# Performance work log

Hardware: AMD Instinct MI355X
Metric: run time of the kernel (lower is better)

The kernel has to match this reference:

```python
import jax, jax.numpy as jnp
import numpy as np

CELL = 4  # 2 ** cell_2_pow, cell_2_pow = 2
EPS = 1e-5


def conv2d(x, w, b):
    # 3x3 conv, padding 1, NCHW / OIHW
    y = jax.lax.conv_general_dilated(
        x, w, window_strides=(1, 1), padding=((1, 1), (1, 1)),
        dimension_numbers=('NCHW', 'OIHW', 'NCHW'))
    return y + b[None, :, None, None]


def setup_inputs() -> dict:
    key = jax.random.key(0)
    ks = jax.random.split(key, 4)
    B, Cc, H, W = 8, 128, 512, 512
    nh, nw = H // CELL, W // CELL  # ctrl spatial must be padded_img / cell_sz
    return dict(
        image_pipe=jax.random.normal(ks[0], (B, 6, H, W), jnp.float32),
        ctrl_pipe=jax.random.normal(ks[1], (B, Cc, nh, nw), jnp.float32),
        w1=jax.random.normal(ks[2], (50, Cc, 3, 3), jnp.float32) * 0.03,
        b1=jnp.zeros((50,), jnp.float32),
        gamma=jnp.ones((50,), jnp.float32),
        beta=jnp.zeros((50,), jnp.float32),
        mean=jnp.zeros((50,), jnp.float32),
        var=jnp.ones((50,), jnp.float32),
        w2=jax.random.normal(ks[3], (18, 50, 3, 3), jnp.float32) * 0.05,
        b2=jnp.zeros((18,), jnp.float32),
    )


def reference(image_pipe, ctrl_pipe, w1, b1, gamma, beta, mean, var, w2, b2):
    cs = CELL
    B, C6, H, W = image_pipe.shape
    # conv_condense: Conv(Cc->50) -> ReLU -> BatchNorm2d(50, inference) -> Conv(50->18)
    h = jax.nn.relu(conv2d(ctrl_pipe, w1, b1))
    scale = gamma * jax.lax.rsqrt(var + EPS)
    h = (h - mean[None, :, None, None]) * scale[None, :, None, None] + beta[None, :, None, None]
    cond = conv2d(h, w2, b2)  # [B, 18, nh, nw]
    nh, nw = cond.shape[-2], cond.shape[-1]

    padH = (-H) % cs
    padW = (-W) % cs
    rH, rW = H + padH, W + padW
    # F.pad(img, (cell, padW+cell, cell, padH+cell)): left/right then top/bottom
    img = jnp.pad(image_pipe, ((0, 0), (0, 0), (cs, padH + cs), (cs, padW + cs)))

    # 9 cell-strided shifted views; torch loop order: i over width (outer), j over height (inner)
    stack = jnp.stack(
        [img[:, :, j * cs:j * cs + rH, i * cs:i * cs + rW]
         for i in range(3) for j in range(3)], axis=-1)  # [B, 6, rH, rW, 9]
    stack = stack.reshape(B, 2, 3, rH, rW, 9)  # 2 groups of 3 channels

    # per-pixel dynamic 9-tap weights, constant within each cs x cs cell
    wts = cond.reshape(B, 2, 9, nh, nw)
    wts = jnp.repeat(jnp.repeat(wts, cs, axis=3), cs, axis=4)  # [B, 2, 9, rH, rW]

    out = jnp.einsum('bgchwk,bgkhw->bgchw', stack, wts)  # weighted neighborhood sum
    out = out.reshape(B, 6, rH, rW)[:, :, :H, :W]
    return out
```

## Files before the change

### kernel.cpp

```cpp
#include <hip/hip_runtime.h>

typedef __attribute__((ext_vector_type(8))) short short8;
typedef __attribute__((ext_vector_type(4))) float floatx4;

__device__ __forceinline__ unsigned short f2bf(float f) {
    union { float f; unsigned int u; } v; v.f = f;
    unsigned int r = (v.u + 0x7fffu + ((v.u >> 16) & 1u)) >> 16;
    return (unsigned short)r;
}

__global__ __launch_bounds__(256) void transpose_kernel(
    const float* __restrict__ ctrl, unsigned short* __restrict__ ctrlT)
{
    __shared__ unsigned short tile[64 * 66];
    const int t = threadIdx.x;
    const int x0 = blockIdx.x * 64, ci0 = blockIdx.y * 64;
    const int b = blockIdx.z >> 7, y = blockIdx.z & 127;
#pragma unroll
    for (int it = 0; it < 4; it++) {
        int ci_l = it * 16 + (t >> 4);
        int x_l = (t & 15) * 4;
        const float4 v = *(const float4*)&ctrl[(((size_t)b * 128 + ci0 + ci_l) * 128 + y) * 128 + x0 + x_l];
        tile[(x_l + 0) * 66 + ci_l] = f2bf(v.x);
        tile[(x_l + 1) * 66 + ci_l] = f2bf(v.y);
        tile[(x_l + 2) * 66 + ci_l] = f2bf(v.z);
        tile[(x_l + 3) * 66 + ci_l] = f2bf(v.w);
    }
    __syncthreads();
#pragma unroll
    for (int it = 0; it < 2; it++) {
        int x_l = it * 32 + (t >> 3);
        int ci_l = (t & 7) * 8;
        const unsigned int* p = (const unsigned int*)&tile[x_l * 66 + ci_l];
        uint4 u = make_uint4(p[0], p[1], p[2], p[3]);
        *(uint4*)&ctrlT[(((size_t)b * 128 + y) * 128 + x0 + x_l) * 128 + ci0 + ci_l] = u;
    }
}

__global__ __launch_bounds__(256) void prep_w_kernel(
    const float* __restrict__ w1, const float* __restrict__ w2,
    unsigned short* __restrict__ w1p, unsigned short* __restrict__ w2p)
{
    int i = blockIdx.x * 256 + threadIdx.x;
    if (i < 4 * 9 * 64 * 32) {
        int ci = i & 31; int t2 = i >> 5; int co = t2 & 63; int t3 = t2 >> 6;
        int tap = t3 % 9; int c4 = t3 / 9;
        float v = 0.f;
        if (co < 50) v = w1[((size_t)co * 128 + c4 * 32 + ci) * 9 + tap];
        w1p[i] = f2bf(v);
    } else {
        int j = i - 4 * 9 * 64 * 32;
        int ci = j & 31; int t2 = j >> 5; int co = t2 & 31; int t3 = t2 >> 5;
        int tap = t3 % 9; int c4 = t3 / 9;
        int cig = c4 * 32 + ci;
        float v = 0.f;
        if (co < 18 && cig < 50) v = w2[((size_t)co * 50 + cig) * 9 + tap];
        w2p[j] = f2bf(v);
    }
}

__global__ __launch_bounds__(256) void conv1_mfma(
    const unsigned short* __restrict__ xT, const unsigned short* __restrict__ w1p,
    const float* __restrict__ b1, const float* __restrict__ gamma,
    const float* __restrict__ beta, const float* __restrict__ mean,
    const float* __restrict__ var, unsigned short* __restrict__ h)
{
    __shared__ unsigned short in_s[324 * 40];
    __shared__ unsigned short w_s[9 * 64 * 40];
    const int tid = threadIdx.x;
    const int x0 = blockIdx.x * 16, y0 = blockIdx.y * 16, b = blockIdx.z;
    const int wid = tid >> 6, lane = tid & 63;
    const int ln = lane & 15, q = lane >> 4;

    floatx4 acc[4][4];
#pragma unroll
    for (int mt = 0; mt < 4; mt++)
#pragma unroll
        for (int nt = 0; nt < 4; nt++) acc[mt][nt] = (floatx4)(0.f);

    uint4 in_r[6], w_r[9];
    auto load_in = [&](int c4) {
#pragma unroll
        for (int k = 0; k < 6; k++) {
            int i = tid + k * 256;
            if (i < 1296) {
                int p = i >> 2, g = i & 3;
                int gy = y0 + p / 18 - 1, gx = x0 + p % 18 - 1;
                in_r[k] = make_uint4(0, 0, 0, 0);
                if (gy >= 0 && gy < 128 && gx >= 0 && gx < 128)
                    in_r[k] = *(const uint4*)&xT[(((size_t)b * 128 + gy) * 128 + gx) * 128 + c4 * 32 + g * 8];
            }
        }
    };
    auto load_w = [&](int c4) {
#pragma unroll
        for (int it = 0; it < 9; it++) {
            int f = it * 256 + tid;
            int g = f & 3, co = (f >> 2) & 63, tap = f >> 8;
            w_r[it] = *(const uint4*)&w1p[(((size_t)c4 * 9 + tap) * 64 + co) * 32 + g * 8];
        }
    };
    auto write_in = [&]() {
#pragma unroll
        for (int k = 0; k < 6; k++) {
            int i = tid + k * 256;
            if (i < 1296) {
                int p = i >> 2, g = i & 3;
                *(uint4*)&in_s[p * 40 + g * 8] = in_r[k];
            }
        }
    };
    auto write_w = [&]() {
#pragma unroll
        for (int it = 0; it < 9; it++) {
            int f = it * 256 + tid;
            int g = f & 3, co = (f >> 2) & 63, tap = f >> 8;
            *(uint4*)&w_s[(tap * 64 + co) * 40 + g * 8] = w_r[it];
        }
    };

    load_in(0); load_w(0);
    write_in(); write_w();
    __syncthreads();

    for (int c4 = 0; c4 < 4; c4++) {
        if (c4 < 3) { load_in(c4 + 1); load_w(c4 + 1); }
#pragma unroll
        for (int tap = 0; tap < 9; tap++) {
            const int dy = tap / 3, dx = tap % 3;
            short8 a[4];
#pragma unroll
            for (int mt = 0; mt < 4; mt++)
                a[mt] = *(const short8*)&in_s[((wid * 4 + mt + dy) * 18 + ln + dx) * 40 + q * 8];
#pragma unroll
            for (int nt = 0; nt < 4; nt++) {
                short8 bf = *(const short8*)&w_s[(tap * 64 + nt * 16 + ln) * 40 + q * 8];
#pragma unroll
                for (int mt = 0; mt < 4; mt++)
                    acc[mt][nt] = __builtin_amdgcn_mfma_f32_16x16x32_bf16(a[mt], bf, acc[mt][nt], 0, 0, 0);
            }
        }
        __syncthreads();
        if (c4 < 3) { write_in(); write_w(); __syncthreads(); }
    }

#pragma unroll
    for (int nt = 0; nt < 4; nt++) {
        int co = nt * 16 + ln;
        bool real = co < 50;
        float sc = 0.f, mn = 0.f, bt = 0.f, bs = 0.f;
        if (real) {
            sc = gamma[co] * rsqrtf(var[co] + 1e-5f);
            mn = mean[co]; bt = beta[co]; bs = b1[co];
        }
#pragma unroll
        for (int mt = 0; mt < 4; mt++) {
            int gy = y0 + wid * 4 + mt;
#pragma unroll
            for (int r = 0; r < 4; r++) {
                int px = q * 4 + r;
                float v = 0.f;
                if (real) {
                    float tv = fmaxf(acc[mt][nt][r] + bs, 0.f);
                    v = (tv - mn) * sc + bt;
                }
                h[(((size_t)b * 128 + gy) * 128 + x0 + px) * 64 + co] = f2bf(v);
            }
        }
    }
}

__global__ __launch_bounds__(256) void conv2_mfma(
    const unsigned short* __restrict__ hT, const unsigned short* __restrict__ w2p,
    const float* __restrict__ b2, float* __restrict__ cond)
{
    __shared__ unsigned short in_s[324 * 40];
    __shared__ unsigned short w_s[2][9 * 32 * 40];
    const int tid = threadIdx.x;
    const int x0 = blockIdx.x * 16, y0 = blockIdx.y * 16, b = blockIdx.z;
    const int wid = tid >> 6, lane = tid & 63;
    const int ln = lane & 15, q = lane >> 4;

    floatx4 acc[4][2];
#pragma unroll
    for (int mt = 0; mt < 4; mt++)
#pragma unroll
        for (int nt = 0; nt < 2; nt++) acc[mt][nt] = (floatx4)(0.f);

    uint4 in_r[6];
    auto load_in = [&](int c4) {
#pragma unroll
        for (int k = 0; k < 6; k++) {
            int i = tid + k * 256;
            if (i < 1296) {
                int p = i >> 2, g = i & 3;
                int gy = y0 + p / 18 - 1, gx = x0 + p % 18 - 1;
                in_r[k] = make_uint4(0, 0, 0, 0);
                if (gy >= 0 && gy < 128 && gx >= 0 && gx < 128)
                    in_r[k] = *(const uint4*)&hT[(((size_t)b * 128 + gy) * 128 + gx) * 64 + c4 * 32 + g * 8];
            }
        }
    };
    auto write_in = [&]() {
#pragma unroll
        for (int k = 0; k < 6; k++) {
            int i = tid + k * 256;
            if (i < 1296) {
                int p = i >> 2, g = i & 3;
                *(uint4*)&in_s[p * 40 + g * 8] = in_r[k];
            }
        }
    };

    load_in(0);
#pragma unroll
    for (int it = 0; it < 9; it++) {
        int f = it * 256 + tid;
        int c4w = f >= 1152 ? 1 : 0;
        int f2 = f - c4w * 1152;
        int g = f2 & 3, co = (f2 >> 2) & 31, tap = f2 >> 7;
        uint4 v = *(const uint4*)&w2p[(((size_t)c4w * 9 + tap) * 32 + co) * 32 + g * 8];
        *(uint4*)&w_s[c4w][(tap * 32 + co) * 40 + g * 8] = v;
    }
    write_in();
    __syncthreads();

    for (int c4 = 0; c4 < 2; c4++) {
        if (c4 < 1) load_in(1);
#pragma unroll
        for (int tap = 0; tap < 9; tap++) {
            const int dy = tap / 3, dx = tap % 3;
            short8 a[4];
#pragma unroll
            for (int mt = 0; mt < 4; mt++)
                a[mt] = *(const short8*)&in_s[((wid * 4 + mt + dy) * 18 + ln + dx) * 40 + q * 8];
#pragma unroll
            for (int nt = 0; nt < 2; nt++) {
                short8 bf = *(const short8*)&w_s[c4][(tap * 32 + nt * 16 + ln) * 40 + q * 8];
#pragma unroll
                for (int mt = 0; mt < 4; mt++)
                    acc[mt][nt] = __builtin_amdgcn_mfma_f32_16x16x32_bf16(a[mt], bf, acc[mt][nt], 0, 0, 0);
            }
        }
        if (c4 < 1) {
            __syncthreads();
            write_in();
            __syncthreads();
        }
    }

#pragma unroll
    for (int nt = 0; nt < 2; nt++) {
        int co = nt * 16 + ln;
        if (co < 18) {
            float bs = b2[co];
            int gch = co / 9, k = co % 9;
            int iw = k / 3, jy = k % 3;
#pragma unroll
            for (int mt = 0; mt < 4; mt++) {
                int gy = y0 + wid * 4 + mt;
#pragma unroll
                for (int r = 0; r < 4; r++) {
                    int px = q * 4 + r;
                    cond[((((size_t)b * 2 + gch) * 128 + gy) * 128 + (x0 + px)) * 12 + jy * 4 + iw]
                        = acc[mt][nt][r] + bs;
                }
            }
        }
    }
}

__global__ __launch_bounds__(256) void apply_kernel(
    const float* __restrict__ img, const float* __restrict__ cond,
    float* __restrict__ out)
{
    const int hwid = blockIdx.x;
    const int lid = (hwid & 7) * 512 + (hwid >> 3);
    const int bx = lid & 1, by = (lid >> 1) & 127, bz = lid >> 8;

    const int tid = threadIdx.x;
    const int xl = tid & 63, s = tid >> 6;
    const int x4 = bx * 64 + xl;
    const int o = by * 4 + s;
    const int b = bz >> 1, g = bz & 1;
    const int xo = x4 * 4;

    const float* cw = &cond[((((size_t)b * 2 + g) * 128 + by) * 128 + x4) * 12];
    float4 w0 = *(const float4*)&cw[0];
    float4 w1 = *(const float4*)&cw[4];
    float4 w2 = *(const float4*)&cw[8];

    float4 C[3][3], L[3][3], R[3][3];
    const bool lok = (x4 > 0), rok_x = (x4 < 127);
#pragma unroll
    for (int jy = 0; jy < 3; jy++) {
        const int r = o - 4 + 4 * jy;
        const bool rk = (r >= 0) && (r < 512);
#pragma unroll
        for (int cc = 0; cc < 3; cc++) {
            C[jy][cc] = make_float4(0.f, 0.f, 0.f, 0.f);
            L[jy][cc] = make_float4(0.f, 0.f, 0.f, 0.f);
            R[jy][cc] = make_float4(0.f, 0.f, 0.f, 0.f);
            if (rk) {
                const float* rp = &img[((((size_t)b * 6 + g * 3 + cc) * 512) + r) * 512];
                C[jy][cc] = *(const float4*)&rp[xo];
                if (lok)   L[jy][cc] = *(const float4*)&rp[xo - 4];
                if (rok_x) R[jy][cc] = *(const float4*)&rp[xo + 4];
            }
        }
    }

    float4 acc[3];
#pragma unroll
    for (int cc = 0; cc < 3; cc++) acc[cc] = make_float4(0.f, 0.f, 0.f, 0.f);

#pragma unroll
    for (int jy = 0; jy < 3; jy++) {
        const float4 wj = (jy == 0) ? w0 : (jy == 1) ? w1 : w2;
#pragma unroll
        for (int cc = 0; cc < 3; cc++) {
            const float4 l = L[jy][cc], c = C[jy][cc], r = R[jy][cc];
            acc[cc].x += l.x * wj.x + c.x * wj.y + r.x * wj.z;
            acc[cc].y += l.y * wj.x + c.y * wj.y + r.y * wj.z;
            acc[cc].z += l.z * wj.x + c.z * wj.y + r.z * wj.z;
            acc[cc].w += l.w * wj.x + c.w * wj.y + r.w * wj.z;
        }
    }

#pragma unroll
    for (int cc = 0; cc < 3; cc++)
        *(float4*)&out[((((size_t)b * 6 + g * 3 + cc) * 512) + o) * 512 + xo] = acc[cc];
}

extern "C" void kernel_launch(void* const* d_in, const int* in_sizes, int n_in,
                              void* d_out, int out_size, void* d_ws, size_t ws_size,
                              hipStream_t stream)
{
    const float* img   = (const float*)d_in[0];
    const float* ctrl  = (const float*)d_in[1];
    const float* w1    = (const float*)d_in[2];
    const float* b1    = (const float*)d_in[3];
    const float* gamma = (const float*)d_in[4];
    const float* beta  = (const float*)d_in[5];
    const float* mean  = (const float*)d_in[6];
    const float* var   = (const float*)d_in[7];
    const float* w2    = (const float*)d_in[8];
    const float* b2    = (const float*)d_in[9];
    float* out = (float*)d_out;

    char* ws = (char*)d_ws;
    unsigned short* ctrlT = (unsigned short*)ws;
    float*          cond  = (float*)ws;
    unsigned short* hbuf  = (unsigned short*)(ws + 33554432);
    unsigned short* w1p   = (unsigned short*)(ws + 50331648);
    unsigned short* w2p   = (unsigned short*)(ws + 50479104);

    transpose_kernel<<<dim3(2, 2, 1024), 256, 0, stream>>>(ctrl, ctrlT);
    prep_w_kernel<<<360, 256, 0, stream>>>(w1, w2, w1p, w2p);
    conv1_mfma<<<dim3(8, 8, 8), 256, 0, stream>>>(ctrlT, w1p, b1, gamma, beta, mean, var, hbuf);
    conv2_mfma<<<dim3(8, 8, 8), 256, 0, stream>>>(hbuf, w2p, b2, cond);
    apply_kernel<<<4096, 256, 0, stream>>>(img, cond, out);
}
```

Baseline: 243.6 us.

## Use direct global-to-LDS loads with pre-padded halo buffers in conv kernels

```diff
diff --git a/kernel.cpp b/kernel.cpp
--- a/kernel.cpp
+++ b/kernel.cpp
@@ -7,6 +7,12 @@
     union { float f; unsigned int u; } v; v.f = f;
     unsigned int r = (v.u + 0x7fffu + ((v.u >> 16) & 1u)) >> 16;
     return (unsigned short)r;
+}
+
+__device__ __forceinline__ void gload_lds16(const void* g, void* l) {
+    __builtin_amdgcn_global_load_lds(
+        (const __attribute__((address_space(1))) unsigned int*)g,
+        (__attribute__((address_space(3))) unsigned int*)l, 16, 0, 0);
 }
 
 __global__ __launch_bounds__(256) void transpose_kernel(
@@ -33,29 +39,50 @@
         int ci_l = (t & 7) * 8;
         const unsigned int* p = (const unsigned int*)&tile[x_l * 66 + ci_l];
         uint4 u = make_uint4(p[0], p[1], p[2], p[3]);
-        *(uint4*)&ctrlT[(((size_t)b * 128 + y) * 128 + x0 + x_l) * 128 + ci0 + ci_l] = u;
+        *(uint4*)&ctrlT[(((size_t)b * 130 + (y + 1)) * 130 + (x0 + x_l + 1)) * 128 + ci0 + ci_l] = u;
     }
 }
 
 __global__ __launch_bounds__(256) void prep_w_kernel(
     const float* __restrict__ w1, const float* __restrict__ w2,
-    unsigned short* __restrict__ w1p, unsigned short* __restrict__ w2p)
+    unsigned short* __restrict__ w1p, unsigned short* __restrict__ w2p,
+    unsigned short* __restrict__ ctrlT, unsigned short* __restrict__ hbuf)
 {
     int i = blockIdx.x * 256 + threadIdx.x;
-    if (i < 4 * 9 * 64 * 32) {
+    if (i < 73728) {
         int ci = i & 31; int t2 = i >> 5; int co = t2 & 63; int t3 = t2 >> 6;
         int tap = t3 % 9; int c4 = t3 / 9;
         float v = 0.f;
         if (co < 50) v = w1[((size_t)co * 128 + c4 * 32 + ci) * 9 + tap];
         w1p[i] = f2bf(v);
-    } else {
-        int j = i - 4 * 9 * 64 * 32;
+    } else if (i < 92160) {
+        int j = i - 73728;
         int ci = j & 31; int t2 = j >> 5; int co = t2 & 31; int t3 = t2 >> 5;
         int tap = t3 % 9; int c4 = t3 / 9;
         int cig = c4 * 32 + ci;
         float v = 0.f;
         if (co < 18 && cig < 50) v = w2[((size_t)co * 50 + cig) * 9 + tap];
         w2p[j] = f2bf(v);
+    } else if (i < 158208) {
+        int k = i - 92160;
+        int b = k / 8256, r = k % 8256;
+        int px = r >> 4, u4 = r & 15;
+        int Y, X;
+        if (px < 130)      { Y = 0;        X = px; }
+        else if (px < 260) { Y = 129;      X = px - 130; }
+        else if (px < 388) { Y = px - 259; X = 0; }
+        else               { Y = px - 387; X = 129; }
+        *(uint4*)&ctrlT[(((size_t)b * 130 + Y) * 130 + X) * 128 + u4 * 8] = make_uint4(0, 0, 0, 0);
+    } else {
+        int k = i - 158208;
+        int b = k / 4128, r = k % 4128;
+        int px = r >> 3, u4 = r & 7;
+        int Y, X;
+        if (px < 130)      { Y = 0;        X = px; }
+        else if (px < 260) { Y = 129;      X = px - 130; }
+        else if (px < 388) { Y = px - 259; X = 0; }
+        else               { Y = px - 387; X = 129; }
+        *(uint4*)&hbuf[(((size_t)b * 130 + Y) * 130 + X) * 64 + u4 * 8] = make_uint4(0, 0, 0, 0);
     }
 }
 
@@ -65,8 +92,8 @@
     const float* __restrict__ beta, const float* __restrict__ mean,
     const float* __restrict__ var, unsigned short* __restrict__ h)
 {
-    __shared__ unsigned short in_s[324 * 40];
-    __shared__ unsigned short w_s[9 * 64 * 40];
+    __shared__ unsigned short in_s[1344 * 8];
+    __shared__ unsigned short w_s[2304 * 8];
     const int tid = threadIdx.x;
     const int x0 = blockIdx.x * 16, y0 = blockIdx.y * 16, b = blockIdx.z;
     const int wid = tid >> 6, lane = tid & 63;
@@ -78,70 +105,42 @@
 #pragma unroll
         for (int nt = 0; nt < 4; nt++) acc[mt][nt] = (floatx4)(0.f);
 
-    uint4 in_r[6], w_r[9];
-    auto load_in = [&](int c4) {
-#pragma unroll
-        for (int k = 0; k < 6; k++) {
-            int i = tid + k * 256;
-            if (i < 1296) {
-                int p = i >> 2, g = i & 3;
-                int gy = y0 + p / 18 - 1, gx = x0 + p % 18 - 1;
-                in_r[k] = make_uint4(0, 0, 0, 0);
-                if (gy >= 0 && gy < 128 && gx >= 0 && gx < 128)
-                    in_r[k] = *(const uint4*)&xT[(((size_t)b * 128 + gy) * 128 + gx) * 128 + c4 * 32 + g * 8];
-            }
-        }
-    };
-    auto load_w = [&](int c4) {
+    for (int c4 = 0; c4 < 4; c4++) {
+#pragma unroll
+        for (int it = 0; it < 6; it++) {
+            const int cbase = it * 256 + wid * 64;
+            if (cbase < 1296) {
+                int j = cbase + lane; if (j > 1295) j = 1295;
+                const int p = j >> 2, s = j & 3;
+                const int Y = y0 + p / 18, X = x0 + p % 18;
+                gload_lds16(&xT[(((size_t)b * 130 + Y) * 130 + X) * 128 + c4 * 32 + s * 8],
+                            &in_s[(size_t)cbase * 8]);
+            }
+        }
+        const unsigned short* wsrc = &w1p[(size_t)c4 * 2304 * 8];
 #pragma unroll
         for (int it = 0; it < 9; it++) {
-            int f = it * 256 + tid;
-            int g = f & 3, co = (f >> 2) & 63, tap = f >> 8;
-            w_r[it] = *(const uint4*)&w1p[(((size_t)c4 * 9 + tap) * 64 + co) * 32 + g * 8];
-        }
-    };
-    auto write_in = [&]() {
-#pragma unroll
-        for (int k = 0; k < 6; k++) {
-            int i = tid + k * 256;
-            if (i < 1296) {
-                int p = i >> 2, g = i & 3;
-                *(uint4*)&in_s[p * 40 + g * 8] = in_r[k];
-            }
-        }
-    };
-    auto write_w = [&]() {
-#pragma unroll
-        for (int it = 0; it < 9; it++) {
-            int f = it * 256 + tid;
-            int g = f & 3, co = (f >> 2) & 63, tap = f >> 8;
-            *(uint4*)&w_s[(tap * 64 + co) * 40 + g * 8] = w_r[it];
-        }
-    };
-
-    load_in(0); load_w(0);
-    write_in(); write_w();
-    __syncthreads();
-
-    for (int c4 = 0; c4 < 4; c4++) {
-        if (c4 < 3) { load_in(c4 + 1); load_w(c4 + 1); }
+            const int cbase = it * 256 + wid * 64;
+            gload_lds16(&wsrc[(size_t)(cbase + lane) * 8], &w_s[(size_t)cbase * 8]);
+        }
+        __syncthreads();
+
 #pragma unroll
         for (int tap = 0; tap < 9; tap++) {
             const int dy = tap / 3, dx = tap % 3;
             short8 a[4];
 #pragma unroll
             for (int mt = 0; mt < 4; mt++)
-                a[mt] = *(const short8*)&in_s[((wid * 4 + mt + dy) * 18 + ln + dx) * 40 + q * 8];
+                a[mt] = *(const short8*)&in_s[(((wid * 4 + mt + dy) * 18 + ln + dx) * 4 + q) * 8];
 #pragma unroll
             for (int nt = 0; nt < 4; nt++) {
-                short8 bf = *(const short8*)&w_s[(tap * 64 + nt * 16 + ln) * 40 + q * 8];
+                short8 bf = *(const short8*)&w_s[((tap * 64 + nt * 16 + ln) * 4 + q) * 8];
 #pragma unroll
                 for (int mt = 0; mt < 4; mt++)
                     acc[mt][nt] = __builtin_amdgcn_mfma_f32_16x16x32_bf16(a[mt], bf, acc[mt][nt], 0, 0, 0);
             }
         }
         __syncthreads();
-        if (c4 < 3) { write_in(); write_w(); __syncthreads(); }
     }
 
 #pragma unroll
@@ -164,7 +163,7 @@
                     float tv = fmaxf(acc[mt][nt][r] + bs, 0.f);
                     v = (tv - mn) * sc + bt;
                 }
-                h[(((size_t)b * 128 + gy) * 128 + x0 + px) * 64 + co] = f2bf(v);
+                h[(((size_t)b * 130 + (gy + 1)) * 130 + (x0 + px + 1)) * 64 + co] = f2bf(v);
             }
         }
     }
@@ -174,8 +173,8 @@
     const unsigned short* __restrict__ hT, const unsigned short* __restrict__ w2p,
     const float* __restrict__ b2, float* __restrict__ cond)
 {
-    __shared__ unsigned short in_s[324 * 40];
-    __shared__ unsigned short w_s[2][9 * 32 * 40];
+    __shared__ unsigned short in_s[1344 * 8];
+    __shared__ unsigned short w_s[1152 * 8];
     const int tid = threadIdx.x;
     const int x0 = blockIdx.x * 16, y0 = blockIdx.y * 16, b = blockIdx.z;
     const int wid = tid >> 6, lane = tid & 63;
@@ -187,66 +186,43 @@
 #pragma unroll
         for (int nt = 0; nt < 2; nt++) acc[mt][nt] = (floatx4)(0.f);
 
-    uint4 in_r[6];
-    auto load_in = [&](int c4) {
-#pragma unroll
-        for (int k = 0; k < 6; k++) {
-            int i = tid + k * 256;
-            if (i < 1296) {
-                int p = i >> 2, g = i & 3;
-                int gy = y0 + p / 18 - 1, gx = x0 + p % 18 - 1;
-                in_r[k] = make_uint4(0, 0, 0, 0);
-                if (gy >= 0 && gy < 128 && gx >= 0 && gx < 128)
-                    in_r[k] = *(const uint4*)&hT[(((size_t)b * 128 + gy) * 128 + gx) * 64 + c4 * 32 + g * 8];
-            }
-        }
-    };
-    auto write_in = [&]() {
-#pragma unroll
-        for (int k = 0; k < 6; k++) {
-            int i = tid + k * 256;
-            if (i < 1296) {
-                int p = i >> 2, g = i & 3;
-                *(uint4*)&in_s[p * 40 + g * 8] = in_r[k];
-            }
-        }
-    };
-
-    load_in(0);
-#pragma unroll
-    for (int it = 0; it < 9; it++) {
-        int f = it * 256 + tid;
-        int c4w = f >= 1152 ? 1 : 0;
-        int f2 = f - c4w * 1152;
-        int g = f2 & 3, co = (f2 >> 2) & 31, tap = f2 >> 7;
-        uint4 v = *(const uint4*)&w2p[(((size_t)c4w * 9 + tap) * 32 + co) * 32 + g * 8];
-        *(uint4*)&w_s[c4w][(tap * 32 + co) * 40 + g * 8] = v;
-    }
-    write_in();
-    __syncthreads();
-
     for (int c4 = 0; c4 < 2; c4++) {
-        if (c4 < 1) load_in(1);
+#pragma unroll
+        for (int it = 0; it < 6; it++) {
+            const int cbase = it * 256 + wid * 64;
+            if (cbase < 1296) {
+                int j = cbase + lane; if (j > 1295) j = 1295;
+                const int p = j >> 2, s = j & 3;
+                const int Y = y0 + p / 18, X = x0 + p % 18;
+                gload_lds16(&hT[(((size_t)b * 130 + Y) * 130 + X) * 64 + c4 * 32 + s * 8],
+                            &in_s[(size_t)cbase * 8]);
+            }
+        }
+        const unsigned short* wsrc = &w2p[(size_t)c4 * 1152 * 8];
+#pragma unroll
+        for (int it = 0; it < 5; it++) {
+            const int cbase = it * 256 + wid * 64;
+            if (cbase < 1152)
+                gload_lds16(&wsrc[(size_t)(cbase + lane) * 8], &w_s[(size_t)cbase * 8]);
+        }
+        __syncthreads();
+
 #pragma unroll
         for (int tap = 0; tap < 9; tap++) {
             const int dy = tap / 3, dx = tap % 3;
             short8 a[4];
 #pragma unroll
             for (int mt = 0; mt < 4; mt++)
-                a[mt] = *(const short8*)&in_s[((wid * 4 + mt + dy) * 18 + ln + dx) * 40 + q * 8];
+                a[mt] = *(const short8*)&in_s[(((wid * 4 + mt + dy) * 18 + ln + dx) * 4 + q) * 8];
 #pragma unroll
             for (int nt = 0; nt < 2; nt++) {
-                short8 bf = *(const short8*)&w_s[c4][(tap * 32 + nt * 16 + ln) * 40 + q * 8];
+                short8 bf = *(const short8*)&w_s[((tap * 32 + nt * 16 + ln) * 4 + q) * 8];
 #pragma unroll
                 for (int mt = 0; mt < 4; mt++)
                     acc[mt][nt] = __builtin_amdgcn_mfma_f32_16x16x32_bf16(a[mt], bf, acc[mt][nt], 0, 0, 0);
             }
         }
-        if (c4 < 1) {
-            __syncthreads();
-            write_in();
-            __syncthreads();
-        }
+        __syncthreads();
     }
 
 #pragma unroll
@@ -350,13 +326,13 @@
 
     char* ws = (char*)d_ws;
     unsigned short* ctrlT = (unsigned short*)ws;
-    float*          cond  = (float*)ws;
-    unsigned short* hbuf  = (unsigned short*)(ws + 33554432);
-    unsigned short* w1p   = (unsigned short*)(ws + 50331648);
-    unsigned short* w2p   = (unsigned short*)(ws + 50479104);
+    unsigned short* hbuf  = (unsigned short*)(ws + 34611200);
+    float*          cond  = (float*)(ws + 51916800);
+    unsigned short* w1p   = (unsigned short*)(ws + 64499712);
+    unsigned short* w2p   = (unsigned short*)(ws + 64647168);
 
     transpose_kernel<<<dim3(2, 2, 1024), 256, 0, stream>>>(ctrl, ctrlT);
-    prep_w_kernel<<<360, 256, 0, stream>>>(w1, w2, w1p, w2p);
+    prep_w_kernel<<<747, 256, 0, stream>>>(w1, w2, w1p, w2p, ctrlT, hbuf);
     conv1_mfma<<<dim3(8, 8, 8), 256, 0, stream>>>(ctrlT, w1p, b1, gamma, beta, mean, var, hbuf);
     conv2_mfma<<<dim3(8, 8, 8), 256, 0, stream>>>(hbuf, w2p, b2, cond);
     apply_kernel<<<4096, 256, 0, stream>>>(img, cond, out);
```

Result: faster. 225.9 us (-7.3%).
